# Kernel optimization log

Hardware: AMD Instinct MI355X
Metric: run time of the kernel (lower is better)

The kernel has to match this reference:

```python
import jax, jax.numpy as jnp
import numpy as np

G, N, DEG = 64, 2048, 8          # graphs, nodes/graph, avg degree
NTOT = G * N                      # 131072 nodes
E = NTOT * DEG                    # 1048576 edges
K = int(np.ceil(0.2 * N))         # 410 nodes kept per graph (SAGPooling ratio=0.2)
NK = G * K                        # 26240 pooled nodes
H, C = 3, 20                      # GAT heads, per-head channels
NEG_BIG = jnp.float32(-1e30)


def gcn(x, src, dst, W, b, n):
    """PyG GCNConv: x' = D^-1/2 (A+I) D^-1/2 x W + b (edge weight 1)."""
    h = x @ W
    deg = jax.ops.segment_sum(jnp.ones(src.shape[0], x.dtype), dst, num_segments=n) + 1.0
    dinv = jax.lax.rsqrt(deg)
    coef = dinv[src] * dinv[dst]                    # [E]
    agg = jax.ops.segment_sum(h[src] * coef[:, None], dst, num_segments=n)
    agg = agg + h * (dinv * dinv)[:, None]          # self loops
    return agg + b


def setup_inputs() -> dict:
    key = jax.random.key(0)
    ks = jax.random.split(key, 16)
    # edges constrained within each graph: per-graph local indices + offsets
    off = jnp.repeat(jnp.arange(G, dtype=jnp.int32) * N, N * DEG)   # [E]
    src = jax.random.randint(ks[0], (E,), 0, N, dtype=jnp.int32) + off
    dst = jax.random.randint(ks[1], (E,), 0, N, dtype=jnp.int32) + off
    batch = jnp.repeat(jnp.arange(G, dtype=jnp.int32), N)           # [NTOT]
    x = jax.random.normal(ks[2], (NTOT, 5), jnp.float32)
    s = 0.1
    return {
        "x": x, "src": src, "dst": dst, "batch": batch,
        "W1": jax.random.normal(ks[3], (5, 10)) * s,   "b1": jnp.zeros((10,)),
        "Ws": jax.random.normal(ks[4], (10, 1)) * s,   "bs": jnp.zeros((1,)),
        "Wg": jax.random.normal(ks[5], (10, H * C)) * s,
        "a_src": jax.random.normal(ks[6], (H, C)) * s,
        "a_dst": jax.random.normal(ks[7], (H, C)) * s,
        "bg": jnp.zeros((H * C,)),
        "Wf1": jax.random.normal(ks[8], (60, 30)) * s, "bf1": jnp.zeros((30,)),
        "Wf2": jax.random.normal(ks[9], (30, 3)) * s,  "bf2": jnp.zeros((3,)),
    }


def reference(x, src, dst, batch, W1, b1, Ws, bs, Wg, a_src, a_dst, bg, Wf1, bf1, Wf2, bf2):
    n = x.shape[0]
    # GCNConv(5,10)
    x1 = gcn(x, src, dst, W1, b1, n)                              # [NTOT,10]
    # SAGPooling: GCN scorer, top-k per graph, gate by tanh(score)
    score = gcn(x1, src, dst, Ws, bs, n)[:, 0]                    # [NTOT]
    _, topi = jax.lax.top_k(score.reshape(G, N), K)               # [G,K]
    perm = (topi + (jnp.arange(G) * N)[:, None]).reshape(-1)      # [NK] global ids
    xp = x1[perm] * jnp.tanh(score[perm])[:, None]                # [NK,10]
    # remap edges; drop (mask) edges touching removed nodes (filter_adj)
    new_idx = jnp.full((n,), -1, jnp.int32).at[perm].set(jnp.arange(NK, dtype=jnp.int32))
    s2, d2 = new_idx[src], new_idx[dst]
    emask = (s2 >= 0) & (d2 >= 0)
    s2 = jnp.where(emask, s2, 0)
    d2 = jnp.where(emask, d2, 0)
    # GATConv(10, 20, heads=3) with self loops
    h = (xp @ Wg).reshape(NK, H, C)
    al_s = jnp.sum(h * a_src, -1)                                 # [NK,H]
    al_d = jnp.sum(h * a_dst, -1)
    loop = jnp.arange(NK, dtype=jnp.int32)
    sa = jnp.concatenate([s2, loop])
    da = jnp.concatenate([d2, loop])
    ma = jnp.concatenate([emask, jnp.ones((NK,), bool)])
    logits = jax.nn.leaky_relu(al_s[sa] + al_d[da], 0.2)          # [E+NK,H]
    logits = jnp.where(ma[:, None], logits, NEG_BIG)
    mx = jax.ops.segment_max(logits, da, num_segments=NK)         # finite: self loops
    w = jnp.exp(logits - mx[da]) * ma[:, None]
    denom = jax.ops.segment_sum(w, da, num_segments=NK)
    alpha = w / denom[da]                                         # edge softmax
    out = jax.ops.segment_sum(h[sa] * alpha[..., None], da, num_segments=NK)  # [NK,H,C]
    xg = out.reshape(NK, H * C) + bg                              # concat heads -> 60
    # scatter_add readout over graphs
    g = jax.ops.segment_sum(xg, batch[perm], num_segments=G)      # [G,60]
    # MLP + LogSoftmax
    z = jax.nn.relu(g @ Wf1 + bf1) @ Wf2 + bf2                    # [G,3]
    return jax.nn.log_softmax(z, axis=1)
```

## Files before the change

kernel.cpp:

```cpp
#include <hip/hip_runtime.h>
#include <math.h>

#define G    64
#define NPG  2048
#define NTOT (G * NPG)
#define EPG  (NPG * 8)
#define KSEL 410
#define NH   3
#define NC   20
#define HC   60
#define FCAP 24
#define KPAD 512
#define RP   12

#define OFF_H1P   0
#define OFF_XP    0
#define OFF_FADJ  16400
#define OFF_FCNT  36080
#define OFF_HF    37728
#define OFF_CSR   98304
#define OFF_HIST  131072
#define OFF_RS    139264
#define OFF_ALS   139264
#define OFF_ALD   144184
#define OFF_SK    147456
#define OFF_WRED  149104
#define OFF_GOUT  151024
#define OFF_HID   151264
#define OFF_NEWL  155648
#define OFF_PERML 159744
#define OFF_WSUM  160568
#define OFF_FLAGS 160632
#define ARENA_SZ  160648

__device__ inline float leaky(float x) { return x >= 0.f ? x : 0.2f * x; }

__device__ inline int wave_incl_scan(int v) {
    int lane = threadIdx.x & 63;
#pragma unroll
    for (int d = 1; d < 64; d <<= 1) {
        int t = __shfl_up(v, d, 64);
        if (lane >= d) v += t;
    }
    return v;
}

__global__ __launch_bounds__(1024) void k_all(
    const float* __restrict__ x, const int* __restrict__ src, const int* __restrict__ dst,
    const float* __restrict__ W1, const float* __restrict__ b1,
    const float* __restrict__ Ws, const float* __restrict__ bs,
    const float* __restrict__ Wg, const float* __restrict__ a_srcw,
    const float* __restrict__ a_dstw, const float* __restrict__ bg,
    const float* __restrict__ Wf1, const float* __restrict__ bf1,
    const float* __restrict__ Wf2, const float* __restrict__ bf2,
    float* __restrict__ out)
{
    __shared__ __align__(16) char arena[ARENA_SZ];
    float*          h1p   = (float*)(arena + OFF_H1P);
    float*          xpL   = (float*)(arena + OFF_XP);
    unsigned short* fadjL = (unsigned short*)(arena + OFF_FADJ);
    int*            fcntL = (int*)(arena + OFF_FCNT);
    float*          hfL   = (float*)(arena + OFF_HF);
    unsigned short* csrL  = (unsigned short*)(arena + OFF_CSR);
    int*            hist  = (int*)(arena + OFF_HIST);
    int*            rsL   = (int*)(arena + OFF_RS);
    float*          alsL  = (float*)(arena + OFF_ALS);
    float*          aldL  = (float*)(arena + OFF_ALD);
    unsigned*       skL   = (unsigned*)(arena + OFF_SK);
    float*          wred  = (float*)(arena + OFF_WRED);
    float*          goutL = (float*)(arena + OFF_GOUT);
    float*          hidL  = (float*)(arena + OFF_HID);
    unsigned short* newLs = (unsigned short*)(arena + OFF_NEWL);
    unsigned short* permL = (unsigned short*)(arena + OFF_PERML);
    int*            wsumL = (int*)(arena + OFF_WSUM);
    int*            flags = (int*)(arena + OFF_FLAGS);
#define bselS  flags[0]
#define bneedS flags[1]
#define totS   flags[3]

    int g = blockIdx.x, tid = threadIdx.x, wid = tid >> 6;
    int nbase = g * NPG, ebase = g * EPG;

    for (int i = tid; i < NPG; i += 1024) hist[i] = 0;
    for (int i = tid; i < NPG; i += 1024) {
        float xi[5];
#pragma unroll
        for (int k = 0; k < 5; k++) xi[k] = x[(size_t)(nbase + i) * 5 + k];
        float v[10];
#pragma unroll
        for (int j = 0; j < 10; j++) {
            float s = 0.f;
#pragma unroll
            for (int k = 0; k < 5; k++) s += xi[k] * W1[k * 10 + j];
            v[j] = s;
        }
        float4* row = (float4*)(h1p + i * RP);
        row[0] = make_float4(v[0], v[1], v[2], v[3]);
        row[1] = make_float4(v[4], v[5], v[6], v[7]);
        row[2] = make_float4(v[8], v[9], 0.f, 0.f);
    }
    __syncthreads();
    for (int e = tid; e < EPG; e += 1024)
        atomicAdd(&hist[dst[ebase + e] - nbase], 1);
    __syncthreads();
    {
        int b2 = tid * 2;
        int v0 = hist[b2], v1 = hist[b2 + 1];
        int s = v0 + v1;
        int incl = wave_incl_scan(s);
        if ((tid & 63) == 63) wsumL[wid] = incl;
        __syncthreads();
        if (tid == 0) {
            int a = 0;
#pragma unroll
            for (int w = 0; w < 16; w++) { int t = wsumL[w]; wsumL[w] = a; a += t; }
        }
        __syncthreads();
        int base = wsumL[wid] + incl - s;
        rsL[b2] = base;
        rsL[b2 + 1] = base + v0;
        h1p[b2 * RP + 10] = rsqrtf((float)v0 + 1.0f);
        h1p[(b2 + 1) * RP + 10] = rsqrtf((float)v1 + 1.0f);
        hist[b2] = 0; hist[b2 + 1] = 0;
    }
    __syncthreads();
    for (int e = tid; e < EPG; e += 1024) {
        int ee = ebase + e;
        int sl = src[ee] - nbase;
        int dl = dst[ee] - nbase;
        int pos = rsL[dl] + atomicAdd(&hist[dl], 1);
        csrL[pos] = (unsigned short)sl;
    }
    __syncthreads();

    {
        int i0 = tid, i1 = tid + 1024;
        int e0 = rsL[i0], e0e = rsL[i0 + 1];
        int e1 = rsL[i1], e1e = (i1 == NPG - 1) ? EPG : rsL[i1 + 1];
        float acc0[10], acc1[10];
#pragma unroll
        for (int j = 0; j < 10; j++) { acc0[j] = 0.f; acc1[j] = 0.f; }
        while (e0 < e0e || e1 < e1e) {
            if (e0 < e0e) {
                int s = csrL[e0++];
                const float4* rw = (const float4*)(h1p + s * RP);
                float4 r0 = rw[0], r1 = rw[1], r2 = rw[2];
                float dv = r2.z;
                acc0[0] += r0.x * dv; acc0[1] += r0.y * dv; acc0[2] += r0.z * dv; acc0[3] += r0.w * dv;
                acc0[4] += r1.x * dv; acc0[5] += r1.y * dv; acc0[6] += r1.z * dv; acc0[7] += r1.w * dv;
                acc0[8] += r2.x * dv; acc0[9] += r2.y * dv;
            }
            if (e1 < e1e) {
                int s = csrL[e1++];
                const float4* rw = (const float4*)(h1p + s * RP);
                float4 r0 = rw[0], r1 = rw[1], r2 = rw[2];
                float dv = r2.z;
                acc1[0] += r0.x * dv; acc1[1] += r0.y * dv; acc1[2] += r0.z * dv; acc1[3] += r0.w * dv;
                acc1[4] += r1.x * dv; acc1[5] += r1.y * dv; acc1[6] += r1.z * dv; acc1[7] += r1.w * dv;
                acc1[8] += r2.x * dv; acc1[9] += r2.y * dv;
            }
        }
        const float4* q0 = (const float4*)(h1p + i0 * RP);
        const float4* q1 = (const float4*)(h1p + i1 * RP);
        float4 s00 = q0[0], s01 = q0[1], s02 = q0[2];
        float4 s10 = q1[0], s11 = q1[1], s12 = q1[2];
        float di0 = s02.z, d20 = di0 * di0;
        float di1 = s12.z, d21 = di1 * di1;
        float b1r[10];
#pragma unroll
        for (int j = 0; j < 10; j++) b1r[j] = b1[j];
        float v0[10], v1[10];
        v0[0] = acc0[0] * di0 + s00.x * d20 + b1r[0];
        v0[1] = acc0[1] * di0 + s00.y * d20 + b1r[1];
        v0[2] = acc0[2] * di0 + s00.z * d20 + b1r[2];
        v0[3] = acc0[3] * di0 + s00.w * d20 + b1r[3];
        v0[4] = acc0[4] * di0 + s01.x * d20 + b1r[4];
        v0[5] = acc0[5] * di0 + s01.y * d20 + b1r[5];
        v0[6] = acc0[6] * di0 + s01.z * d20 + b1r[6];
        v0[7] = acc0[7] * di0 + s01.w * d20 + b1r[7];
        v0[8] = acc0[8] * di0 + s02.x * d20 + b1r[8];
        v0[9] = acc0[9] * di0 + s02.y * d20 + b1r[9];
        v1[0] = acc1[0] * di1 + s10.x * d21 + b1r[0];
        v1[1] = acc1[1] * di1 + s10.y * d21 + b1r[1];
        v1[2] = acc1[2] * di1 + s10.z * d21 + b1r[2];
        v1[3] = acc1[3] * di1 + s10.w * d21 + b1r[3];
        v1[4] = acc1[4] * di1 + s11.x * d21 + b1r[4];
        v1[5] = acc1[5] * di1 + s11.y * d21 + b1r[5];
        v1[6] = acc1[6] * di1 + s11.z * d21 + b1r[6];
        v1[7] = acc1[7] * di1 + s11.w * d21 + b1r[7];
        v1[8] = acc1[8] * di1 + s12.x * d21 + b1r[8];
        v1[9] = acc1[9] * di1 + s12.y * d21 + b1r[9];
        float hs0 = 0.f, hs1 = 0.f;
#pragma unroll
        for (int j = 0; j < 10; j++) { float w = Ws[j]; hs0 += v0[j] * w; hs1 += v1[j] * w; }
        __syncthreads();
        float4* w0 = (float4*)(h1p + i0 * RP);
        w0[0] = make_float4(v0[0], v0[1], v0[2], v0[3]);
        w0[1] = make_float4(v0[4], v0[5], v0[6], v0[7]);
        w0[2] = make_float4(v0[8], v0[9], di0, hs0);
        float4* w1 = (float4*)(h1p + i1 * RP);
        w1[0] = make_float4(v1[0], v1[1], v1[2], v1[3]);
        w1[1] = make_float4(v1[4], v1[5], v1[6], v1[7]);
        w1[2] = make_float4(v1[8], v1[9], di1, hs1);
    }
    __syncthreads();

    {
        float bsv = bs[0];
        int i0 = tid, i1 = tid + 1024;
        float2 own0 = *(const float2*)(h1p + i0 * RP + 10);
        float2 own1 = *(const float2*)(h1p + i1 * RP + 10);
        int e0 = rsL[i0], e0e = rsL[i0 + 1];
        int e1 = rsL[i1], e1e = (i1 == NPG - 1) ? EPG : rsL[i1 + 1];
        float a0 = 0.f, a1 = 0.f;
        while (e0 < e0e || e1 < e1e) {
            if (e0 < e0e) { float2 dh = *(const float2*)(h1p + csrL[e0++] * RP + 10); a0 += dh.x * dh.y; }
            if (e1 < e1e) { float2 dh = *(const float2*)(h1p + csrL[e1++] * RP + 10); a1 += dh.x * dh.y; }
        }
        float sc0 = own0.x * a0 + own0.y * own0.x * own0.x + bsv;
        float sc1 = own1.x * a1 + own1.y * own1.x * own1.x + bsv;
        unsigned u0 = __float_as_uint(sc0);
        unsigned u1 = __float_as_uint(sc1);
        skL[i0] = (u0 & 0x80000000u) ? ~u0 : (u0 | 0x80000000u);
        skL[i1] = (u1 & 0x80000000u) ? ~u1 : (u1 | 0x80000000u);
        newLs[i0] = 0xFFFFu; newLs[i1] = 0xFFFFu;
        hist[i0] = 0; hist[i1] = 0;
    }
    int need = KSEL;
    unsigned prefix = 0;
    __syncthreads();

    for (int lv = 0; lv < 3; lv++) {
        for (int i = tid; i < NPG; i += 1024) {
            unsigned k = skL[i];
            bool match; unsigned bb;
            if (lv == 0)      { match = true;                  bb = k >> 21; }
            else if (lv == 1) { match = ((k >> 21) == prefix); bb = (k >> 10) & 0x7FFu; }
            else              { match = ((k >> 10) == prefix); bb = k & 0x3FFu; }
            if (match) atomicAdd(&hist[bb], 1);
        }
        __syncthreads();
        int b2 = tid * 2;
        int v0 = hist[b2], v1 = hist[b2 + 1];
        hist[b2] = 0; hist[b2 + 1] = 0;
        int s = v0 + v1;
        int incl = wave_incl_scan(s);
        if ((tid & 63) == 63) wsumL[wid] = incl;
        __syncthreads();
        if (tid == 0) {
            int a = 0;
#pragma unroll
            for (int w = 0; w < 16; w++) { int t = wsumL[w]; wsumL[w] = a; a += t; }
            totS = a;
        }
        __syncthreads();
        int base = wsumL[wid] + incl - s;
        int tot = totS;
        { int Sb = tot - base;        int Sb1 = Sb - v0; if (Sb >= need && Sb1 < need) { bselS = b2;     bneedS = need - Sb1; } }
        { int Sb = tot - (base + v0); int Sb1 = Sb - v1; if (Sb >= need && Sb1 < need) { bselS = b2 + 1; bneedS = need - Sb1; } }
        __syncthreads();
        if (lv == 0)      prefix = (unsigned)bselS;
        else if (lv == 1) prefix = (prefix << 11) | (unsigned)bselS;
        else              prefix = (prefix << 10) | (unsigned)bselS;
        need = bneedS;
        __syncthreads();
    }
    unsigned T = prefix;
    int greaterCnt = KSEL - need;

    {
        int b2 = tid * 2;
        unsigned k0 = skL[b2], k1 = skL[b2 + 1];
        int gt0 = k0 > T ? 1 : 0, gt1 = k1 > T ? 1 : 0;
        int eq0 = k0 == T ? 1 : 0, eq1 = k1 == T ? 1 : 0;
        int pack = ((gt0 + gt1) << 16) | (eq0 + eq1);
        int incl = wave_incl_scan(pack);
        if ((tid & 63) == 63) wsumL[wid] = incl;
        __syncthreads();
        if (tid == 0) {
            int a = 0;
#pragma unroll
            for (int w = 0; w < 16; w++) { int t = wsumL[w]; wsumL[w] = a; a += t; }
        }
        __syncthreads();
        int base = wsumL[wid] + incl - pack;
        int gb = base >> 16, eb = base & 0xFFFF;
        if (gt0) { permL[gb] = (unsigned short)b2; newLs[b2] = (unsigned short)gb; }
        if (gt1) { int r = gb + gt0; permL[r] = (unsigned short)(b2 + 1); newLs[b2 + 1] = (unsigned short)r; }
        if (eq0 && eb < need) { int p = greaterCnt + eb; permL[p] = (unsigned short)b2; newLs[b2] = (unsigned short)p; }
        if (eq1) { int r = eb + eq0; if (r < need) { int p = greaterCnt + r; permL[p] = (unsigned short)(b2 + 1); newLs[b2 + 1] = (unsigned short)p; } }
    }
    __syncthreads();

    {
        float4 rq0, rq1, rq2; float tt = 0.f;
        bool havep = (tid < KSEL);
        if (havep) {
            int iL = permL[tid];
            unsigned k = skL[iL];
            unsigned u = (k & 0x80000000u) ? (k & 0x7FFFFFFFu) : ~k;
            tt = tanhf(__uint_as_float(u));
            const float4* xr = (const float4*)(h1p + iL * RP);
            rq0 = xr[0]; rq1 = xr[1]; rq2 = xr[2];
        }
        __syncthreads();
        if (havep) {
            float* xp = xpL + tid * 10;
            xp[0] = rq0.x * tt; xp[1] = rq0.y * tt; xp[2] = rq0.z * tt; xp[3] = rq0.w * tt;
            xp[4] = rq1.x * tt; xp[5] = rq1.y * tt; xp[6] = rq1.z * tt; xp[7] = rq1.w * tt;
            xp[8] = rq2.x * tt; xp[9] = rq2.y * tt;
        }
    }
    __syncthreads();

    for (int p = tid; p < KSEL; p += 1024) {
        int iL = permL[p];
        int p0 = rsL[iL], p1 = (iL == NPG - 1) ? EPG : rsL[iL + 1];
        int c = 0;
        int e = p0;
        while (e < p1) {
            int n = p1 - e; n = n > 8 ? 8 : n;
            int b8[8];
#pragma unroll
            for (int j = 0; j < 8; j++) b8[j] = csrL[e + (j < n ? j : 0)];
            unsigned short n8[8];
#pragma unroll
            for (int j = 0; j < 8; j++) n8[j] = newLs[b8[j]];
#pragma unroll
            for (int j = 0; j < 8; j++)
                if (j < n && n8[j] != 0xFFFFu && c < FCAP) fadjL[p * FCAP + c++] = n8[j];
            e += n;
        }
        fcntL[p] = c;
    }
    __syncthreads();

    for (int t = tid; t < KSEL * NH; t += 1024) {
        int p = t / NH, hh = t - p * NH;
        float xi[10];
#pragma unroll
        for (int k = 0; k < 10; k++) xi[k] = xpL[p * 10 + k];
        float v[NC];
        float as_ = 0.f, ad_ = 0.f;
#pragma unroll
        for (int c = 0; c < NC; c++) {
            int j = hh * NC + c;
            float vv = 0.f;
#pragma unroll
            for (int k = 0; k < 10; k++) vv += xi[k] * Wg[k * HC + j];
            v[c] = vv;
            as_ += vv * a_srcw[j];
            ad_ += vv * a_dstw[j];
        }
        float4* hr = (float4*)(hfL + p * HC + hh * NC);
#pragma unroll
        for (int q = 0; q < 5; q++)
            hr[q] = make_float4(v[4 * q], v[4 * q + 1], v[4 * q + 2], v[4 * q + 3]);
        alsL[p * NH + hh] = as_;
        aldL[p * NH + hh] = ad_;
    }
    __syncthreads();

    {
        float res[NC];
#pragma unroll
        for (int rnd = 0; rnd < 2; rnd++) {
            int task = rnd == 0 ? tid : 1024 + tid;
            bool on = rnd == 0 || tid < KPAD;
            int hh = task >> 9, p = task & (KPAD - 1);
            if (on) {
                if (p < KSEL) {
                    float aldp = aldL[p * NH + hh];
                    float lself = leaky(alsL[p * NH + hh] + aldp);
                    int c = fcntL[p];
                    const float4* hp = (const float4*)(hfL + p * HC + hh * NC);
                    float4 r0 = hp[0], r1 = hp[1], r2 = hp[2], r3 = hp[3], r4 = hp[4];
                    float wsum = 1.f;
#pragma unroll
                    for (int e = 0; e < FCAP; e++) {
                        if (e < c) {
                            int idx = fadjL[p * FCAP + e];
                            float w = __expf(leaky(alsL[idx * NH + hh] + aldp) - lself);
                            wsum += w;
                            const float4* hq = (const float4*)(hfL + idx * HC + hh * NC);
                            float4 t0 = hq[0], t1 = hq[1], t2 = hq[2], t3 = hq[3], t4 = hq[4];
                            r0.x += w * t0.x; r0.y += w * t0.y; r0.z += w * t0.z; r0.w += w * t0.w;
                            r1.x += w * t1.x; r1.y += w * t1.y; r1.z += w * t1.z; r1.w += w * t1.w;
                            r2.x += w * t2.x; r2.y += w * t2.y; r2.z += w * t2.z; r2.w += w * t2.w;
                            r3.x += w * t3.x; r3.y += w * t3.y; r3.z += w * t3.z; r3.w += w * t3.w;
                            r4.x += w * t4.x; r4.y += w * t4.y; r4.z += w * t4.z; r4.w += w * t4.w;
                        }
                    }
                    float inv = 1.f / wsum;
                    res[0] = r0.x * inv;  res[1] = r0.y * inv;  res[2] = r0.z * inv;  res[3] = r0.w * inv;
                    res[4] = r1.x * inv;  res[5] = r1.y * inv;  res[6] = r1.z * inv;  res[7] = r1.w * inv;
                    res[8] = r2.x * inv;  res[9] = r2.y * inv;  res[10] = r2.z * inv; res[11] = r2.w * inv;
                    res[12] = r3.x * inv; res[13] = r3.y * inv; res[14] = r3.z * inv; res[15] = r3.w * inv;
                    res[16] = r4.x * inv; res[17] = r4.y * inv; res[18] = r4.z * inv; res[19] = r4.w * inv;
                } else {
#pragma unroll
                    for (int cc = 0; cc < NC; cc++) res[cc] = 0.f;
                }
#pragma unroll
                for (int cc = 0; cc < NC; cc++) {
                    float v = res[cc];
#pragma unroll
                    for (int d = 1; d < 64; d <<= 1) v += __shfl_xor(v, d, 64);
                    res[cc] = v;
                }
                if ((tid & 63) == 0) {
                    int slot = rnd == 0 ? hh * 8 + (wid & 7) : 16 + wid;
#pragma unroll
                    for (int cc = 0; cc < NC; cc++) wred[slot * NC + cc] = res[cc];
                }
            }
        }
    }
    __syncthreads();
    if (tid < HC) {
        int hh = tid / NC, c = tid - hh * NC;
        float a = 0.f;
#pragma unroll
        for (int w = 0; w < 8; w++) a += wred[(hh * 8 + w) * NC + c];
        goutL[tid] = a + (float)KSEL * bg[tid];
    }
    __syncthreads();

    if (tid < 30) {
        float s = bf1[tid];
#pragma unroll
        for (int k = 0; k < HC; k++) s += goutL[k] * Wf1[k * 30 + tid];
        hidL[tid] = s > 0.f ? s : 0.f;
    }
    __syncthreads();
    if (tid == 0) {
        float z[3];
#pragma unroll
        for (int j = 0; j < 3; j++) {
            float s = bf2[j];
            for (int k = 0; k < 30; k++) s += hidL[k] * Wf2[k * 3 + j];
            z[j] = s;
        }
        float m = fmaxf(z[0], fmaxf(z[1], z[2]));
        float lse = logf(expf(z[0] - m) + expf(z[1] - m) + expf(z[2] - m)) + m;
#pragma unroll
        for (int j = 0; j < 3; j++) out[g * 3 + j] = z[j] - lse;
    }
}

extern "C" void kernel_launch(void* const* d_in, const int* in_sizes, int n_in,
                              void* d_out, int out_size, void* d_ws, size_t ws_size,
                              hipStream_t stream) {
    const float* x     = (const float*)d_in[0];
    const int*   src   = (const int*)d_in[1];
    const int*   dst   = (const int*)d_in[2];
    const float* W1    = (const float*)d_in[4];
    const float* b1    = (const float*)d_in[5];
    const float* Ws    = (const float*)d_in[6];
    const float* bs    = (const float*)d_in[7];
    const float* Wg    = (const float*)d_in[8];
    const float* a_src = (const float*)d_in[9];
    const float* a_dst = (const float*)d_in[10];
    const float* bg    = (const float*)d_in[11];
    const float* Wf1   = (const float*)d_in[12];
    const float* bf1   = (const float*)d_in[13];
    const float* Wf2   = (const float*)d_in[14];
    const float* bf2   = (const float*)d_in[15];
    float* out = (float*)d_out;
    (void)d_ws; (void)ws_size;

    k_all<<<G, 1024, 0, stream>>>(x, src, dst, W1, b1, Ws, bs, Wg, a_src, a_dst,
                                  bg, Wf1, bf1, Wf2, bf2, out);
}
```

Before: 141.4 us.

## Drop serial wave-sum scans, precompute score products, and roll GAT edge loop

Replaces the single-thread cross-wave prefix loops, and the barriers around them, with each thread summing the 16 wave totals itself. It precomputes hs*dinv per node into a compact array so the score gather reads one float instead of a float2. It also turns the fully unrolled FCAP GAT loop into a dynamic loop bounded by the neighbour count, and adds a launch-bounds occupancy hint. The aim is fewer block-wide barriers, less LDS traffic and less register pressure, at the cost of an extra barrier before the histogram clear and redundant per-thread LDS reads.

```diff
diff --git a/kernel.cpp b/kernel.cpp
--- a/kernel.cpp
+++ b/kernel.cpp
@@ -45,7 +45,7 @@
     return v;
 }
 
-__global__ __launch_bounds__(1024) void k_all(
+__global__ __launch_bounds__(1024, 4) void k_all(
     const float* __restrict__ x, const int* __restrict__ src, const int* __restrict__ dst,
     const float* __restrict__ W1, const float* __restrict__ b1,
     const float* __restrict__ Ws, const float* __restrict__ bs,
@@ -63,6 +63,7 @@
     float*          hfL   = (float*)(arena + OFF_HF);
     unsigned short* csrL  = (unsigned short*)(arena + OFF_CSR);
     int*            hist  = (int*)(arena + OFF_HIST);
+    float*          prB   = (float*)(arena + OFF_HIST);
     int*            rsL   = (int*)(arena + OFF_RS);
     float*          alsL  = (float*)(arena + OFF_ALS);
     float*          aldL  = (float*)(arena + OFF_ALD);
@@ -76,7 +77,6 @@
     int*            flags = (int*)(arena + OFF_FLAGS);
 #define bselS  flags[0]
 #define bneedS flags[1]
-#define totS   flags[3]
 
     int g = blockIdx.x, tid = threadIdx.x, wid = tid >> 6;
     int nbase = g * NPG, ebase = g * EPG;
@@ -110,13 +110,10 @@
         int incl = wave_incl_scan(s);
         if ((tid & 63) == 63) wsumL[wid] = incl;
         __syncthreads();
-        if (tid == 0) {
-            int a = 0;
-#pragma unroll
-            for (int w = 0; w < 16; w++) { int t = wsumL[w]; wsumL[w] = a; a += t; }
-        }
-        __syncthreads();
-        int base = wsumL[wid] + incl - s;
+        int pre = 0;
+#pragma unroll
+        for (int w = 0; w < 16; w++) { int t = wsumL[w]; if (w < wid) pre += t; }
+        int base = pre + incl - s;
         rsL[b2] = base;
         rsL[b2 + 1] = base + v0;
         h1p[b2 * RP + 10] = rsqrtf((float)v0 + 1.0f);
@@ -202,6 +199,8 @@
         w1[0] = make_float4(v1[0], v1[1], v1[2], v1[3]);
         w1[1] = make_float4(v1[4], v1[5], v1[6], v1[7]);
         w1[2] = make_float4(v1[8], v1[9], di1, hs1);
+        prB[i0] = hs0 * di0;
+        prB[i1] = hs1 * di1;
     }
     __syncthreads();
 
@@ -214,8 +213,8 @@
         int e1 = rsL[i1], e1e = (i1 == NPG - 1) ? EPG : rsL[i1 + 1];
         float a0 = 0.f, a1 = 0.f;
         while (e0 < e0e || e1 < e1e) {
-            if (e0 < e0e) { float2 dh = *(const float2*)(h1p + csrL[e0++] * RP + 10); a0 += dh.x * dh.y; }
-            if (e1 < e1e) { float2 dh = *(const float2*)(h1p + csrL[e1++] * RP + 10); a1 += dh.x * dh.y; }
+            if (e0 < e0e) a0 += prB[csrL[e0++]];
+            if (e1 < e1e) a1 += prB[csrL[e1++]];
         }
         float sc0 = own0.x * a0 + own0.y * own0.x * own0.x + bsv;
         float sc1 = own1.x * a1 + own1.y * own1.x * own1.x + bsv;
@@ -224,10 +223,11 @@
         skL[i0] = (u0 & 0x80000000u) ? ~u0 : (u0 | 0x80000000u);
         skL[i1] = (u1 & 0x80000000u) ? ~u1 : (u1 | 0x80000000u);
         newLs[i0] = 0xFFFFu; newLs[i1] = 0xFFFFu;
-        hist[i0] = 0; hist[i1] = 0;
     }
     int need = KSEL;
     unsigned prefix = 0;
+    __syncthreads();
+    for (int i = tid; i < NPG; i += 1024) hist[i] = 0;
     __syncthreads();
 
     for (int lv = 0; lv < 3; lv++) {
@@ -247,15 +247,10 @@
         int incl = wave_incl_scan(s);
         if ((tid & 63) == 63) wsumL[wid] = incl;
         __syncthreads();
-        if (tid == 0) {
-            int a = 0;
-#pragma unroll
-            for (int w = 0; w < 16; w++) { int t = wsumL[w]; wsumL[w] = a; a += t; }
-            totS = a;
-        }
-        __syncthreads();
-        int base = wsumL[wid] + incl - s;
-        int tot = totS;
+        int pre = 0, tot = 0;
+#pragma unroll
+        for (int w = 0; w < 16; w++) { int t = wsumL[w]; if (w < wid) pre += t; tot += t; }
+        int base = pre + incl - s;
         { int Sb = tot - base;        int Sb1 = Sb - v0; if (Sb >= need && Sb1 < need) { bselS = b2;     bneedS = need - Sb1; } }
         { int Sb = tot - (base + v0); int Sb1 = Sb - v1; if (Sb >= need && Sb1 < need) { bselS = b2 + 1; bneedS = need - Sb1; } }
         __syncthreads();
@@ -263,7 +258,6 @@
         else if (lv == 1) prefix = (prefix << 11) | (unsigned)bselS;
         else              prefix = (prefix << 10) | (unsigned)bselS;
         need = bneedS;
-        __syncthreads();
     }
     unsigned T = prefix;
     int greaterCnt = KSEL - need;
@@ -277,13 +271,10 @@
         int incl = wave_incl_scan(pack);
         if ((tid & 63) == 63) wsumL[wid] = incl;
         __syncthreads();
-        if (tid == 0) {
-            int a = 0;
-#pragma unroll
-            for (int w = 0; w < 16; w++) { int t = wsumL[w]; wsumL[w] = a; a += t; }
-        }
-        __syncthreads();
-        int base = wsumL[wid] + incl - pack;
+        int pre = 0;
+#pragma unroll
+        for (int w = 0; w < 16; w++) { int t = wsumL[w]; if (w < wid) pre += t; }
+        int base = pre + incl - pack;
         int gb = base >> 16, eb = base & 0xFFFF;
         if (gt0) { permL[gb] = (unsigned short)b2; newLs[b2] = (unsigned short)gb; }
         if (gt1) { int r = gb + gt0; permL[r] = (unsigned short)(b2 + 1); newLs[b2 + 1] = (unsigned short)r; }
@@ -376,20 +367,17 @@
                     const float4* hp = (const float4*)(hfL + p * HC + hh * NC);
                     float4 r0 = hp[0], r1 = hp[1], r2 = hp[2], r3 = hp[3], r4 = hp[4];
                     float wsum = 1.f;
-#pragma unroll
-                    for (int e = 0; e < FCAP; e++) {
-                        if (e < c) {
-                            int idx = fadjL[p * FCAP + e];
-                            float w = __expf(leaky(alsL[idx * NH + hh] + aldp) - lself);
-                            wsum += w;
-                            const float4* hq = (const float4*)(hfL + idx * HC + hh * NC);
-                            float4 t0 = hq[0], t1 = hq[1], t2 = hq[2], t3 = hq[3], t4 = hq[4];
-                            r0.x += w * t0.x; r0.y += w * t0.y; r0.z += w * t0.z; r0.w += w * t0.w;
-                            r1.x += w * t1.x; r1.y += w * t1.y; r1.z += w * t1.z; r1.w += w * t1.w;
-                            r2.x += w * t2.x; r2.y += w * t2.y; r2.z += w * t2.z; r2.w += w * t2.w;
-                            r3.x += w * t3.x; r3.y += w * t3.y; r3.z += w * t3.z; r3.w += w * t3.w;
-                            r4.x += w * t4.x; r4.y += w * t4.y; r4.z += w * t4.z; r4.w += w * t4.w;
-                        }
+                    for (int e = 0; e < c; e++) {
+                        int idx = fadjL[p * FCAP + e];
+                        float w = __expf(leaky(alsL[idx * NH + hh] + aldp) - lself);
+                        wsum += w;
+                        const float4* hq = (const float4*)(hfL + idx * HC + hh * NC);
+                        float4 t0 = hq[0], t1 = hq[1], t2 = hq[2], t3 = hq[3], t4 = hq[4];
+                        r0.x += w * t0.x; r0.y += w * t0.y; r0.z += w * t0.z; r0.w += w * t0.w;
+                        r1.x += w * t1.x; r1.y += w * t1.y; r1.z += w * t1.z; r1.w += w * t1.w;
+                        r2.x += w * t2.x; r2.y += w * t2.y; r2.z += w * t2.z; r2.w += w * t2.w;
+                        r3.x += w * t3.x; r3.y += w * t3.y; r3.z += w * t3.z; r3.w += w * t3.w;
+                        r4.x += w * t4.x; r4.y += w * t4.y; r4.z += w * t4.z; r4.w += w * t4.w;
                     }
                     float inv = 1.f / wsum;
                     res[0] = r0.x * inv;  res[1] = r0.y * inv;  res[2] = r0.z * inv;  res[3] = r0.w * inv;
```

After: 141.7 us. About the same (+0.2%).
